# Performance work log

Hardware: AMD Instinct MI355X
Metric: run time of the kernel (lower is better)

## Reference

```python
import jax, jax.numpy as jnp
import numpy as np

H, DK, DV, D = 16, 64, 64, 1024  # num_heads, q/k size, v size, embedding_dim


def setup_inputs() -> dict:
    key = jax.random.key(0)
    k1, k2, k3, k4 = jax.random.split(key, 4)
    scale = 1.0 / np.sqrt(D)
    X = jax.random.normal(k1, (4, 2048, D), dtype=jnp.float32)
    # stacked per-head projection weights (one Linear per head in the original ModuleList)
    Wq = jax.random.normal(k2, (H, D, DK), dtype=jnp.float32) * scale
    Wk = jax.random.normal(k3, (H, D, DK), dtype=jnp.float32) * scale
    Wv = jax.random.normal(k4, (H, D, DV), dtype=jnp.float32) * scale
    return {"X": X, "Wq": Wq, "Wk": Wk, "Wv": Wv}


def reference(X, Wq, Wk, Wv):
    # Batched equivalent of looping over per-head attention layers and concatenating.
    q = jnp.einsum("bsd,hde->bhse", X, Wq)  # [B,H,S,DK]
    k = jnp.einsum("bsd,hde->bhse", X, Wk)  # [B,H,S,DK]
    v = jnp.einsum("bsd,hde->bhse", X, Wv)  # [B,H,S,DV]
    scores = jnp.einsum("bhqe,bhke->bhqk", q, k) / jnp.sqrt(jnp.asarray(DK, q.dtype))
    attn = jax.nn.softmax(scores, axis=-1)
    out = jnp.einsum("bhqk,bhke->bhqe", attn, v)  # [B,H,S,DV]
    B, _, S, _ = out.shape
    # concat over heads along last dim (head order preserved)
    return out.transpose(0, 2, 1, 3).reshape(B, S, H * DV)
```

## Files before the change

### kernel.cpp

```cpp
#include <hip/hip_runtime.h>
#include <hip/hip_bf16.h>
#include <stdint.h>

typedef __attribute__((ext_vector_type(8))) short bf16x8;
typedef __attribute__((ext_vector_type(4))) float f32x4;
typedef __attribute__((ext_vector_type(16))) float f32x16;

__device__ __forceinline__ unsigned short f2bf(float f) {
  union { float f; unsigned u; } v; v.f = f;
  unsigned r = (v.u + 0x7FFFu + ((v.u >> 16) & 1u)) >> 16;
  return (unsigned short)r;
}

__device__ __forceinline__ float fexp2(float x) {
#if __has_builtin(__builtin_amdgcn_exp2f)
  return __builtin_amdgcn_exp2f(x);
#else
  float r; asm("v_exp_f32 %0, %1" : "=v"(r) : "v"(x)); return r;
#endif
}

__device__ __forceinline__ void gload16(const void* g, void* l) {
  __builtin_amdgcn_global_load_lds(
      (const __attribute__((address_space(1))) void*)g,
      (__attribute__((address_space(3))) void*)l, 16, 0, 0);
}

__device__ __forceinline__ bf16x8 lds_read8(const unsigned short* base, int row, int k0) {
  int byteoff = row * 128 + (((k0 >> 3) ^ (row & 7)) << 4);
  return *(const bf16x8*)((const char*)base + byteoff);
}

__device__ __forceinline__ bf16x8 lds_at(const unsigned short* smem, unsigned off) {
  return *(const bf16x8*)((const char*)smem + off);
}

__device__ __forceinline__ unsigned int cvtpk(float a, float b) {
  unsigned int r;
  asm("v_cvt_pk_bf16_f32 %0, %1, %2" : "=v"(r) : "v"(a), "v"(b));
  return r;
}

__global__ void cvt_x_kernel(const float* __restrict__ X, unsigned short* __restrict__ Xb) {
  int i = blockIdx.x * blockDim.x + threadIdx.x;
  const float4* src = (const float4*)X;
  float4 a = src[2 * i];
  float4 b = src[2 * i + 1];
  bf16x8 o;
  o[0] = (short)f2bf(a.x); o[1] = (short)f2bf(a.y);
  o[2] = (short)f2bf(a.z); o[3] = (short)f2bf(a.w);
  o[4] = (short)f2bf(b.x); o[5] = (short)f2bf(b.y);
  o[6] = (short)f2bf(b.z); o[7] = (short)f2bf(b.w);
  *(bf16x8*)(Xb + (size_t)i * 8) = o;
}

__global__ void cvt_w_kernel(const float* __restrict__ Wq, const float* __restrict__ Wk,
                             const float* __restrict__ Wv, unsigned short* __restrict__ Wbt) {
  __shared__ float t[64][65];
  const int k0 = blockIdx.x * 64;
  const int h  = blockIdx.y;
  const int p  = blockIdx.z;
  const float* W = (p == 0 ? Wq : (p == 1 ? Wk : Wv)) + (size_t)h * 1024 * 64;
  const int tid = threadIdx.x;
  {
    int e = tid & 63, kq = tid >> 6;
#pragma unroll
    for (int i = 0; i < 16; ++i) {
      int k = i * 4 + kq;
      t[k][e] = W[(size_t)(k0 + k) * 64 + e];
    }
  }
  __syncthreads();
  {
    int k = tid & 63, eq = tid >> 6;
#pragma unroll
    for (int i = 0; i < 16; ++i) {
      int e = i * 4 + eq;
      Wbt[(size_t)((p * 1024) + h * 64 + e) * 1024 + k0 + k] = f2bf(t[k][e]);
    }
  }
}

__global__ __launch_bounds__(256, 3) void proj_gemm(
    const unsigned short* __restrict__ Xb,
    const unsigned short* __restrict__ Wbt,
    unsigned short* __restrict__ Qb,
    unsigned short* __restrict__ Kb,
    unsigned short* __restrict__ Vt) {
  __shared__ unsigned short As[128 * 64];
  __shared__ unsigned short Bs[128 * 64];
  const int m0 = blockIdx.x * 128;
  const int n0 = blockIdx.y * 128;
  const int tid = threadIdx.x;
  const int lane = tid & 63;
  const int wid = tid >> 6;
  const int wr = wid >> 1, wc = wid & 1;

  const unsigned short* Ag = Xb + (size_t)m0 * 1024;
  const unsigned short* Bg = Wbt + (size_t)n0 * 1024;

  f32x4 acc[4][4];
#pragma unroll
  for (int i = 0; i < 4; ++i)
#pragma unroll
    for (int j = 0; j < 4; ++j) acc[i][j] = (f32x4){0.f, 0.f, 0.f, 0.f};

  for (int kt = 0; kt < 16; ++kt) {
#pragma unroll
    for (int i = 0; i < 4; ++i) {
      int row0 = wid * 32 + i * 8;
      int lr = row0 + (lane >> 3);
      int slot = (lane & 7) ^ (lr & 7);
      gload16(Ag + (size_t)lr * 1024 + kt * 64 + slot * 8, (char*)As + row0 * 128);
      gload16(Bg + (size_t)lr * 1024 + kt * 64 + slot * 8, (char*)Bs + row0 * 128);
    }
    __syncthreads();
#pragma unroll
    for (int ks = 0; ks < 2; ++ks) {
      int k0 = ks * 32 + (lane >> 4) * 8;
      bf16x8 a[4], b[4];
#pragma unroll
      for (int mi = 0; mi < 4; ++mi) a[mi] = lds_read8(As, wr * 64 + mi * 16 + (lane & 15), k0);
#pragma unroll
      for (int ni = 0; ni < 4; ++ni) b[ni] = lds_read8(Bs, wc * 64 + ni * 16 + (lane & 15), k0);
#pragma unroll
      for (int mi = 0; mi < 4; ++mi)
#pragma unroll
        for (int ni = 0; ni < 4; ++ni)
          acc[mi][ni] = __builtin_amdgcn_mfma_f32_16x16x32_bf16(a[mi], b[ni], acc[mi][ni], 0, 0, 0);
    }
    __syncthreads();
  }

#pragma unroll
  for (int mi = 0; mi < 4; ++mi) {
    int m = m0 + wr * 64 + mi * 16 + ((lane >> 4) << 2);
    int bb = m >> 11;
    int s  = m & 2047;
#pragma unroll
    for (int ni = 0; ni < 4; ++ni) {
      int n = n0 + wc * 64 + ni * 16 + (lane & 15);
      int p = n >> 10;
      int h = (n >> 6) & 15, e = n & 63;
#pragma unroll
      for (int r = 0; r < 4; ++r) {
        float v = acc[mi][ni][r];
        int sr = s + r;
        if (p == 0) {
          Qb[((size_t)(bb * 16 + h) * 2048 + sr) * 64 + e] = f2bf(v * 0.18033688f);
        } else if (p == 1) {
          Kb[((size_t)(bb * 16 + h) * 2048 + sr) * 64 + e] = f2bf(v);
        } else {
          int spos = (sr & ~12) | ((sr & 4) << 1) | ((sr & 8) >> 1);
          Vt[((size_t)(bb * 16 + h) * 64 + e) * 2048 + spos] = f2bf(v);
        }
      }
    }
  }
}

__global__ __launch_bounds__(256, 2) void attn_kernel(
    const unsigned short* __restrict__ Qb,
    const unsigned short* __restrict__ Kb,
    const unsigned short* __restrict__ Vt,
    float* __restrict__ out) {
  __shared__ unsigned short smem[16384];
  const int bh = blockIdx.x;
  const int q0 = blockIdx.y * 256;
  const int tid = threadIdx.x;
  const int lane = tid & 63;
  const int wid = tid >> 6;
  const int ql = lane & 31;
  const int hi = lane >> 5;

  const unsigned short* Qp = Qb + (size_t)bh * 2048 * 64;
  const unsigned short* Kp = Kb + (size_t)bh * 2048 * 64;
  const unsigned short* Vp = Vt + (size_t)bh * 64 * 2048;

  bf16x8 qf0[4], qf1[4];
#pragma unroll
  for (int ks = 0; ks < 4; ++ks) {
    qf0[ks] = *(const bf16x8*)(Qp + (size_t)(q0 + wid * 64 + ql) * 64 + ks * 16 + hi * 8);
    qf1[ks] = *(const bf16x8*)(Qp + (size_t)(q0 + wid * 64 + 32 + ql) * 64 + ks * 16 + hi * 8);
  }

  f32x16 a00, a01, a10, a11;
#pragma unroll
  for (int i = 0; i < 16; ++i) { a00[i] = 0.f; a01[i] = 0.f; a10[i] = 0.f; a11[i] = 0.f; }
  float l0 = 0.f, l1 = 0.f;

  const unsigned lane_off = (unsigned)(ql * 128 + (((ql & 7) ^ hi) << 4));

  auto STAGE = [&](int buf, int kt) {
    unsigned short* Ks = smem + buf * 8192;
    unsigned short* Vs = Ks + 4096;
#pragma unroll
    for (int i = 0; i < 2; ++i) {
      int row0 = wid * 16 + i * 8;
      int lr = row0 + (lane >> 3);
      int slot = (lane & 7) ^ (lr & 7);
      gload16(Kp + (size_t)(kt * 64 + lr) * 64 + slot * 8, (char*)Ks + row0 * 128);
      gload16(Vp + (size_t)lr * 2048 + kt * 64 + slot * 8, (char*)Vs + row0 * 128);
    }
  };

  STAGE(0, 0);
  asm volatile("s_waitcnt vmcnt(0)" ::: "memory");
  __builtin_amdgcn_s_barrier();

  int cur = 0;
  for (int kt = 0; kt < 32; ++kt) {
    if (kt < 31) STAGE(cur ^ 1, kt + 1);
    const unsigned cb = (unsigned)cur << 14;

#pragma unroll
    for (int t = 0; t < 2; ++t) {
      bf16x8 kf[4];
#pragma unroll
      for (int ks = 0; ks < 4; ++ks)
        kf[ks] = lds_at(smem, lane_off ^ (cb | (t << 12) | (ks << 5)));

      f32x16 s0, s1;
#pragma unroll
      for (int i = 0; i < 16; ++i) { s0[i] = 0.f; s1[i] = 0.f; }
#pragma unroll
      for (int ks = 0; ks < 4; ++ks) {
        s0 = __builtin_amdgcn_mfma_f32_32x32x16_bf16(kf[ks], qf0[ks], s0, 0, 0, 0);
        s1 = __builtin_amdgcn_mfma_f32_32x32x16_bf16(kf[ks], qf1[ks], s1, 0, 0, 0);
      }

#pragma unroll
      for (int i = 0; i < 16; ++i) { s0[i] = fexp2(s0[i]); s1[i] = fexp2(s1[i]); }

      {
        float sm0[8], sm1[8];
#pragma unroll
        for (int i = 0; i < 8; ++i) { sm0[i] = s0[i] + s0[i + 8]; sm1[i] = s1[i] + s1[i + 8]; }
        l0 += ((sm0[0] + sm0[1]) + (sm0[2] + sm0[3])) + ((sm0[4] + sm0[5]) + (sm0[6] + sm0[7]));
        l1 += ((sm1[0] + sm1[1]) + (sm1[2] + sm1[3])) + ((sm1[4] + sm1[5]) + (sm1[6] + sm1[7]));
      }

      union { unsigned int u[4]; bf16x8 v; } P00, P01, P10, P11;
#pragma unroll
      for (int j = 0; j < 4; ++j) {
        P00.u[j] = cvtpk(s0[2 * j],     s0[2 * j + 1]);
        P01.u[j] = cvtpk(s0[8 + 2 * j], s0[8 + 2 * j + 1]);
        P10.u[j] = cvtpk(s1[2 * j],     s1[2 * j + 1]);
        P11.u[j] = cvtpk(s1[8 + 2 * j], s1[8 + 2 * j + 1]);
      }

      bf16x8 vf00 = lds_at(smem, lane_off ^ (cb | 8192u | (0 << 12) | (t << 6) | (0 << 5)));
      bf16x8 vf01 = lds_at(smem, lane_off ^ (cb | 8192u | (0 << 12) | (t << 6) | (1 << 5)));
      bf16x8 vf10 = lds_at(smem, lane_off ^ (cb | 8192u | (1 << 12) | (t << 6) | (0 << 5)));
      bf16x8 vf11 = lds_at(smem, lane_off ^ (cb | 8192u | (1 << 12) | (t << 6) | (1 << 5)));

      a00 = __builtin_amdgcn_mfma_f32_32x32x16_bf16(vf00, P00.v, a00, 0, 0, 0);
      a10 = __builtin_amdgcn_mfma_f32_32x32x16_bf16(vf00, P10.v, a10, 0, 0, 0);
      a00 = __builtin_amdgcn_mfma_f32_32x32x16_bf16(vf01, P01.v, a00, 0, 0, 0);
      a10 = __builtin_amdgcn_mfma_f32_32x32x16_bf16(vf01, P11.v, a10, 0, 0, 0);
      a01 = __builtin_amdgcn_mfma_f32_32x32x16_bf16(vf10, P00.v, a01, 0, 0, 0);
      a11 = __builtin_amdgcn_mfma_f32_32x32x16_bf16(vf10, P10.v, a11, 0, 0, 0);
      a01 = __builtin_amdgcn_mfma_f32_32x32x16_bf16(vf11, P01.v, a01, 0, 0, 0);
      a11 = __builtin_amdgcn_mfma_f32_32x32x16_bf16(vf11, P11.v, a11, 0, 0, 0);
    }

    asm volatile("s_waitcnt vmcnt(0)" ::: "memory");
    __builtin_amdgcn_s_barrier();
    cur ^= 1;
  }

  __builtin_amdgcn_s_barrier();

  const int b = bh >> 4, h = bh & 15;
  float* fs = (float*)smem + wid * 2048;

#pragma unroll
  for (int g = 0; g < 2; ++g) {
    float lg = g ? l1 : l0;
    float lf = lg + __shfl_xor(lg, 32, 64);
    float inv = 1.0f / lf;
    const f32x16& m0v = g ? a10 : a00;
    const f32x16& m1v = g ? a11 : a01;
#pragma unroll
    for (int r = 0; r < 16; ++r) {
      int e0 = (r & 3) + 8 * (r >> 2) + 4 * hi;
      fs[ql * 64 + (e0 ^ ql)] = m0v[r] * inv;
      int e1 = 32 + e0;
      fs[ql * 64 + (e1 ^ ql)] = m1v[r] * inv;
    }
#pragma unroll
    for (int i = 0; i < 32; ++i) {
      float v = fs[i * 64 + (lane ^ i)];
      out[((size_t)(b * 2048 + q0 + wid * 64 + g * 32 + i)) * 1024 + h * 64 + lane] = v;
    }
  }
}

extern "C" void kernel_launch(void* const* d_in, const int* in_sizes, int n_in,
                              void* d_out, int out_size, void* d_ws, size_t ws_size,
                              hipStream_t stream) {
  (void)in_sizes; (void)n_in; (void)out_size; (void)ws_size;
  const float* X  = (const float*)d_in[0];
  const float* Wq = (const float*)d_in[1];
  const float* Wk = (const float*)d_in[2];
  const float* Wv = (const float*)d_in[3];
  float* out = (float*)d_out;

  unsigned short* Xb  = (unsigned short*)d_ws;
  unsigned short* Wbt = Xb + (size_t)8192 * 1024;
  unsigned short* Qb  = Wbt + (size_t)3 * 1024 * 1024;
  unsigned short* Kb  = Qb + (size_t)64 * 2048 * 64;
  unsigned short* Vt  = Kb + (size_t)64 * 2048 * 64;

  hipLaunchKernelGGL(cvt_x_kernel, dim3(4096), dim3(256), 0, stream, X, Xb);
  hipLaunchKernelGGL(cvt_w_kernel, dim3(16, 16, 3), dim3(256), 0, stream, Wq, Wk, Wv, Wbt);
  hipLaunchKernelGGL(proj_gemm, dim3(64, 24), dim3(256), 0, stream, Xb, Wbt, Qb, Kb, Vt);
  hipLaunchKernelGGL(attn_kernel, dim3(64, 8), dim3(256), 0, stream, Qb, Kb, Vt, out);
}
```

Before: 145.9 us.

## Split attention over the key dimension and add a combine kernel

The attention kernel gains a grid z-dimension that splits the 32 key tiles into two halves. Each half writes unnormalized partial outputs and row sums to workspace, and a new combine kernel adds the two halves and normalizes. The aim is more blocks in flight for better CU utilization. In exchange it adds an extra full-size fp32 output buffer, extra global traffic, and an additional kernel launch. The split only turns on when the workspace is large enough.

Result: slower. 167.1 us (+14.5%).

```diff
diff --git a/kernel.cpp b/kernel.cpp
--- a/kernel.cpp
+++ b/kernel.cpp
@@ -163,10 +163,16 @@
     const unsigned short* __restrict__ Qb,
     const unsigned short* __restrict__ Kb,
     const unsigned short* __restrict__ Vt,
-    float* __restrict__ out) {
+    float* __restrict__ O0,
+    float* __restrict__ O1,
+    float* __restrict__ lpart,
+    int NT) {
   __shared__ unsigned short smem[16384];
   const int bh = blockIdx.x;
   const int q0 = blockIdx.y * 256;
+  const int koff = blockIdx.z;
+  const int kt0 = koff * NT;
+  float* Op = koff ? O1 : O0;
   const int tid = threadIdx.x;
   const int lane = tid & 63;
   const int wid = tid >> 6;
@@ -204,13 +210,13 @@
     }
   };
 
-  STAGE(0, 0);
+  STAGE(0, kt0);
   asm volatile("s_waitcnt vmcnt(0)" ::: "memory");
   __builtin_amdgcn_s_barrier();
 
   int cur = 0;
-  for (int kt = 0; kt < 32; ++kt) {
-    if (kt < 31) STAGE(cur ^ 1, kt + 1);
+  for (int kt = kt0; kt < kt0 + NT; ++kt) {
+    if (kt < kt0 + NT - 1) STAGE(cur ^ 1, kt + 1);
     const unsigned cb = (unsigned)cur << 14;
 
 #pragma unroll
@@ -278,28 +284,54 @@
   for (int g = 0; g < 2; ++g) {
     float lg = g ? l1 : l0;
     float lf = lg + __shfl_xor(lg, 32, 64);
-    float inv = 1.0f / lf;
+    if (hi == 0)
+      lpart[((size_t)koff * 64 + bh) * 2048 + q0 + wid * 64 + g * 32 + ql] = lf;
     const f32x16& m0v = g ? a10 : a00;
     const f32x16& m1v = g ? a11 : a01;
 #pragma unroll
     for (int r = 0; r < 16; ++r) {
       int e0 = (r & 3) + 8 * (r >> 2) + 4 * hi;
-      fs[ql * 64 + (e0 ^ ql)] = m0v[r] * inv;
+      fs[ql * 64 + (e0 ^ ql)] = m0v[r];
       int e1 = 32 + e0;
-      fs[ql * 64 + (e1 ^ ql)] = m1v[r] * inv;
+      fs[ql * 64 + (e1 ^ ql)] = m1v[r];
     }
 #pragma unroll
     for (int i = 0; i < 32; ++i) {
       float v = fs[i * 64 + (lane ^ i)];
-      out[((size_t)(b * 2048 + q0 + wid * 64 + g * 32 + i)) * 1024 + h * 64 + lane] = v;
-    }
+      Op[((size_t)(b * 2048 + q0 + wid * 64 + g * 32 + i)) * 1024 + h * 64 + lane] = v;
+    }
+  }
+}
+
+__global__ void combine_kernel(float* __restrict__ out,
+                               const float* __restrict__ O1,
+                               const float* __restrict__ lpart,
+                               int nsplit) {
+  const size_t n4 = (size_t)8 * 1024 * 1024 / 4;
+  size_t i4 = (size_t)blockIdx.x * blockDim.x + threadIdx.x;
+  for (; i4 < n4; i4 += (size_t)gridDim.x * blockDim.x) {
+    size_t i = i4 * 4;
+    int b = (int)(i >> 21);
+    int s = (int)(i >> 10) & 2047;
+    int h = (int)(i >> 6) & 15;
+    int bh = b * 16 + h;
+    float l = lpart[(size_t)bh * 2048 + s];
+    float4 v = ((const float4*)out)[i4];
+    if (nsplit == 2) {
+      float4 w = ((const float4*)O1)[i4];
+      v.x += w.x; v.y += w.y; v.z += w.z; v.w += w.w;
+      l += lpart[(size_t)64 * 2048 + (size_t)bh * 2048 + s];
+    }
+    float inv = 1.0f / l;
+    v.x *= inv; v.y *= inv; v.z *= inv; v.w *= inv;
+    ((float4*)out)[i4] = v;
   }
 }
 
 extern "C" void kernel_launch(void* const* d_in, const int* in_sizes, int n_in,
                               void* d_out, int out_size, void* d_ws, size_t ws_size,
                               hipStream_t stream) {
-  (void)in_sizes; (void)n_in; (void)out_size; (void)ws_size;
+  (void)in_sizes; (void)n_in; (void)out_size;
   const float* X  = (const float*)d_in[0];
   const float* Wq = (const float*)d_in[1];
   const float* Wk = (const float*)d_in[2];
@@ -311,9 +343,18 @@
   unsigned short* Qb  = Wbt + (size_t)3 * 1024 * 1024;
   unsigned short* Kb  = Qb + (size_t)64 * 2048 * 64;
   unsigned short* Vt  = Kb + (size_t)64 * 2048 * 64;
+  float* O1 = (float*)(Vt + (size_t)64 * 2048 * 64);
+  float* lpart = (float*)Xb;
+
+  const size_t NEED2 = 73400320ull + (size_t)8 * 1024 * 1024 * 4;
+  const int nsplit = (ws_size >= NEED2) ? 2 : 1;
+  const int NT = 32 / nsplit;
 
   hipLaunchKernelGGL(cvt_x_kernel, dim3(4096), dim3(256), 0, stream, X, Xb);
   hipLaunchKernelGGL(cvt_w_kernel, dim3(16, 16, 3), dim3(256), 0, stream, Wq, Wk, Wv, Wbt);
   hipLaunchKernelGGL(proj_gemm, dim3(64, 24), dim3(256), 0, stream, Xb, Wbt, Qb, Kb, Vt);
-  hipLaunchKernelGGL(attn_kernel, dim3(64, 8), dim3(256), 0, stream, Qb, Kb, Vt, out);
-}
+  hipLaunchKernelGGL(attn_kernel, dim3(64, 8, nsplit), dim3(256), 0, stream,
+                     Qb, Kb, Vt, out, O1, lpart, NT);
+  hipLaunchKernelGGL(combine_kernel, dim3(4096), dim3(256), 0, stream,
+                     out, O1, lpart, nsplit);
+}
```
